# Kernel tuning notes

Hardware: AMD Instinct MI355X
Metric: run time of the kernel (lower is better)

## Reference

```python
import jax, jax.numpy as jnp
import numpy as np

N_NODES = 50000
N_EDGES = 800000
IN_DIM = 128
HIDDEN = 32
NHEAD = 4
OUT_DIM = 64
NEG_SLOPE = 0.2


def setup_inputs() -> dict:
    key = jax.random.key(0)
    ks = jax.random.split(key, 8)
    x = jax.random.normal(ks[0], (N_NODES, IN_DIM), dtype=jnp.float32)
    edge_index = jax.random.randint(ks[1], (2, N_EDGES), 0, N_NODES, dtype=jnp.int64)
    # layer 1: fc (in_dim -> nhead*hidden), attn [nhead, 2*hidden]
    W1 = jax.random.normal(ks[2], (IN_DIM, NHEAD * HIDDEN), dtype=jnp.float32) * 0.1
    attn1 = jax.random.normal(ks[3], (NHEAD, 2 * HIDDEN), dtype=jnp.float32) * 0.1
    # layer 2: fc (nhead*hidden -> 1*out_dim), attn [1, 2*out_dim]
    W2 = jax.random.normal(ks[4], (NHEAD * HIDDEN, OUT_DIM), dtype=jnp.float32) * 0.1
    attn2 = jax.random.normal(ks[5], (1, 2 * OUT_DIM), dtype=jnp.float32) * 0.1
    # extra output head: Linear(out_dim, out_dim) with bias
    head_W = jax.random.normal(ks[6], (OUT_DIM, OUT_DIM), dtype=jnp.float32) * 0.1
    head_b = jax.random.normal(ks[7], (OUT_DIM,), dtype=jnp.float32) * 0.1
    return {"x": x, "edge_index": edge_index, "W1": W1, "attn1": attn1,
            "W2": W2, "attn2": attn2, "head_W": head_W, "head_b": head_b}


def _gat_layer(x, W, attn, row, col, num_nodes, heads):
    """One GATConv: linear proj, edge attention, segment softmax over dst (col), scatter-add."""
    f_out = W.shape[1] // heads
    h = (x @ W).reshape(num_nodes, heads, f_out)            # [N, H, F]
    a_l, a_r = attn[:, :f_out], attn[:, f_out:]              # split attn for src/dst parts
    e_src = jnp.einsum('nhf,hf->nh', h, a_l)                 # [N, H]
    e_dst = jnp.einsum('nhf,hf->nh', h, a_r)                 # [N, H]
    alpha = e_src[row] + e_dst[col]                          # [E, H] == cat(h[row],h[col])·attn
    alpha = jax.nn.leaky_relu(alpha, NEG_SLOPE)
    # segment softmax grouped by destination node (col); self-loops guarantee non-empty segs
    amax = jax.ops.segment_max(alpha, col, num_segments=num_nodes)
    ex = jnp.exp(alpha - amax[col])
    denom = jax.ops.segment_sum(ex, col, num_segments=num_nodes)
    a = ex / denom[col]                                      # [E, H]
    msg = h[row] * a[:, :, None]                             # [E, H, F]
    out = jax.ops.segment_sum(msg, col, num_segments=num_nodes)  # [N, H, F]
    return out.reshape(num_nodes, heads * f_out)


def reference(x, edge_index, W1, attn1, W2, attn2, head_W, head_b):
    n = x.shape[0]
    loops = jnp.arange(n, dtype=edge_index.dtype)
    row = jnp.concatenate([edge_index[0], loops])
    col = jnp.concatenate([edge_index[1], loops])
    h = _gat_layer(x, W1, attn1, row, col, n, NHEAD)         # [N, NHEAD*HIDDEN]
    h = jax.nn.relu(h)                                       # intermediate-layer activation
    h = _gat_layer(h, W2, attn2, row, col, n, 1)             # [N, OUT_DIM] (last: no act)
    out = h @ head_W + head_b                                # extra_output_fc head
    return out
```

## Files before the change

### kernel.cpp

```cpp
#include <hip/hip_runtime.h>
#include <math.h>

#define N_NODES 50000
#define E_RAW 800000
#define E_TOT 850000
#define NEG_SLOPE 0.2f
#define G1_BLOCKS ((N_NODES + 63) / 64)
#define NBUCK 391
#define EPB 2048
#define PBLK ((E_TOT + EPB - 1) / EPB)

typedef __attribute__((ext_vector_type(8))) short bf16x8;
typedef __attribute__((ext_vector_type(4))) float f32x4;

__device__ __forceinline__ float lrelu(float a) { return a > 0.f ? a : NEG_SLOPE * a; }

__device__ __forceinline__ unsigned f2bf(float f) {
    unsigned u = __float_as_uint(f);
    return (u + 0x7fff + ((u >> 16) & 1)) >> 16;
}
__device__ __forceinline__ unsigned pack2(float a, float b) {
    return f2bf(a) | (f2bf(b) << 16);
}
__device__ __forceinline__ float bflo(unsigned p) { return __uint_as_float(p << 16); }
__device__ __forceinline__ float bfhi(unsigned p) { return __uint_as_float(p & 0xffff0000u); }

__global__ void k_prepB(const float* __restrict__ W, unsigned* __restrict__ Btg) {
    int c = blockIdx.x;
    int tq = threadIdx.x;
    float a = W[(2 * tq) * 128 + c];
    float b = W[(2 * tq + 1) * 128 + c];
    Btg[c * 64 + tq] = pack2(a, b);
}

__global__ void k_gemm1_p1(const float* __restrict__ A, const unsigned* __restrict__ Btg,
                           const float* __restrict__ aux, uint2* __restrict__ C,
                           float* __restrict__ es, float* __restrict__ ed,
                           const int* __restrict__ ei, int* __restrict__ hist2d) {
    __shared__ unsigned As[64 * 64];
    if (blockIdx.x >= G1_BLOCKS) {
        int blk = blockIdx.x - G1_BLOCKS;
        int* h = (int*)As;
        for (int i = threadIdx.x; i < NBUCK; i += 256) h[i] = 0;
        __syncthreads();
        int base = blk * EPB;
        for (int i = threadIdx.x; i < EPB; i += 256) {
            int e = base + i;
            if (e >= E_TOT) break;
            int col = (e < E_RAW) ? ei[E_RAW + e] : (e - E_RAW);
            atomicAdd(&h[col >> 7], 1);
        }
        __syncthreads();
        for (int i = threadIdx.x; i < NBUCK; i += 256) hist2d[i * PBLK + blk] = h[i];
        return;
    }
    int t = threadIdx.x;
    int m0 = blockIdx.x * 64;
    int rows = min(64, N_NODES - m0);
    const float4* A4 = (const float4*)(A + (size_t)m0 * 128);
    for (int i = t; i < rows * 32; i += 256) {
        int row = i >> 5, k4 = i & 31;
        float4 v = A4[i];
        int byte = (k4 * 8) ^ ((row & 7) << 4);
        unsigned* p = &As[row * 64 + (byte >> 2)];
        p[0] = pack2(v.x, v.y);
        p[1] = pack2(v.z, v.w);
    }
    __syncthreads();
    int lane = t & 63, wave = t >> 6;
    int r15 = lane & 15, g = lane >> 4;
    int arow = wave * 16 + r15;
    f32x4 acc[8];
#pragma unroll
    for (int i = 0; i < 8; ++i) acc[i] = (f32x4){0.f, 0.f, 0.f, 0.f};
    const char* Abase = (const char*)As + arow * 256;
    int swz = (arow & 7) << 4;
    const char* Bbase = (const char*)Btg;
#pragma unroll
    for (int s = 0; s < 4; ++s) {
        bf16x8 xf = *(const bf16x8*)(Abase + ((64 * s + 16 * g) ^ swz));
#pragma unroll
        for (int tt = 0; tt < 8; ++tt) {
            bf16x8 wf = *(const bf16x8*)(Bbase + ((16 * tt + r15) * 256 + 64 * s + 16 * g));
            acc[tt] = __builtin_amdgcn_mfma_f32_16x16x32_bf16(wf, xf, acc[tt], 0, 0, 0);
        }
    }
    int grow = m0 + arow;
    bool valid = (arow < rows);
    if (valid) {
        uint2* C2 = C + (size_t)grow * 32;
#pragma unroll
        for (int tt = 0; tt < 8; ++tt) {
            uint2 v; v.x = pack2(acc[tt][0], acc[tt][1]); v.y = pack2(acc[tt][2], acc[tt][3]);
            C2[4 * tt + g] = v;
        }
    }
    float ps0 = 0.f, ps1 = 0.f, ps2 = 0.f, ps3 = 0.f;
    float pd0 = 0.f, pd1 = 0.f, pd2 = 0.f, pd3 = 0.f;
#pragma unroll
    for (int tt = 0; tt < 8; ++tt) {
        int h = tt >> 1;
        int fin = 16 * (tt & 1) + 4 * g;
        float4 alv = *(const float4*)(aux + h * 64 + fin);
        float4 arv = *(const float4*)(aux + h * 64 + 32 + fin);
        float s4 = acc[tt][0] * alv.x + acc[tt][1] * alv.y + acc[tt][2] * alv.z + acc[tt][3] * alv.w;
        float d4 = acc[tt][0] * arv.x + acc[tt][1] * arv.y + acc[tt][2] * arv.z + acc[tt][3] * arv.w;
        if (h == 0) { ps0 += s4; pd0 += d4; }
        else if (h == 1) { ps1 += s4; pd1 += d4; }
        else if (h == 2) { ps2 += s4; pd2 += d4; }
        else { ps3 += s4; pd3 += d4; }
    }
#pragma unroll
    for (int mask = 16; mask <= 32; mask <<= 1) {
        ps0 += __shfl_xor(ps0, mask); ps1 += __shfl_xor(ps1, mask);
        ps2 += __shfl_xor(ps2, mask); ps3 += __shfl_xor(ps3, mask);
        pd0 += __shfl_xor(pd0, mask); pd1 += __shfl_xor(pd1, mask);
        pd2 += __shfl_xor(pd2, mask); pd3 += __shfl_xor(pd3, mask);
    }
    if (valid) {
        float psg = (g == 0) ? ps0 : (g == 1) ? ps1 : (g == 2) ? ps2 : ps3;
        float pdg = (g == 0) ? pd0 : (g == 1) ? pd1 : (g == 2) ? pd2 : pd3;
        es[grow * 4 + g] = psg;
        ed[grow * 4 + g] = pdg;
    }
}

__global__ void k_p2a(const int* __restrict__ hist2d, int* __restrict__ off2d,
                      int* __restrict__ bucktot) {
    __shared__ int sh[512];
    int b = blockIdx.x, t = threadIdx.x;
    int v = (t < PBLK) ? hist2d[b * PBLK + t] : 0;
    sh[t] = v;
    __syncthreads();
    for (int ofs = 1; ofs < 512; ofs <<= 1) {
        int u = (t >= ofs) ? sh[t - ofs] : 0;
        __syncthreads();
        sh[t] += u;
        __syncthreads();
    }
    if (t < PBLK) off2d[b * PBLK + t] = sh[t] - v;
    if (t == 511) bucktot[b] = sh[511];
}

__global__ void k_p2b(const int* __restrict__ bucktot, int* __restrict__ bucketbase) {
    __shared__ int sh[512];
    int t = threadIdx.x;
    int v = (t < NBUCK) ? bucktot[t] : 0;
    sh[t] = v;
    __syncthreads();
    for (int ofs = 1; ofs < 512; ofs <<= 1) {
        int u = (t >= ofs) ? sh[t - ofs] : 0;
        __syncthreads();
        sh[t] += u;
        __syncthreads();
    }
    if (t < NBUCK) bucketbase[t] = sh[t] - v;
    if (t == 511) bucketbase[NBUCK] = sh[511];
}

__global__ void k_p3(const int* __restrict__ ei, const int* __restrict__ off2d,
                     const int* __restrict__ bucketbase, unsigned* __restrict__ part) {
    __shared__ int h[NBUCK];
    __shared__ int basebuf[NBUCK];
    int blk = blockIdx.x, t = threadIdx.x;
    for (int i = t; i < NBUCK; i += 256) {
        h[i] = 0;
        basebuf[i] = bucketbase[i] + off2d[i * PBLK + blk];
    }
    __syncthreads();
    int base = blk * EPB;
    for (int i = t; i < EPB; i += 256) {
        int e = base + i;
        if (e >= E_TOT) break;
        int col, src;
        if (e < E_RAW) { col = ei[E_RAW + e]; src = ei[e]; }
        else { col = src = e - E_RAW; }
        int b = col >> 7;
        int lr = atomicAdd(&h[b], 1);
        part[basebuf[b] + lr] = (unsigned)src | ((unsigned)(col & 127) << 16);
    }
}

__global__ void k_p4(const unsigned* __restrict__ part, const int* __restrict__ bucketbase,
                     int* __restrict__ off, unsigned short* __restrict__ srcs) {
    __shared__ int h[128];
    __shared__ int colofs[128];
    int b = blockIdx.x, t = threadIdx.x;
    int s0 = bucketbase[b], s1 = bucketbase[b + 1];
    if (t < 128) h[t] = 0;
    __syncthreads();
    for (int i = s0 + t; i < s1; i += 256) atomicAdd(&h[part[i] >> 16], 1);
    __syncthreads();
    if (t == 0) {
        int acc = 0;
        for (int c = 0; c < 128; ++c) { colofs[c] = acc; acc += h[c]; }
    }
    __syncthreads();
    int colbase = b * 128, ncols = min(128, N_NODES - colbase);
    if (t < ncols) off[colbase + t] = s0 + colofs[t];
    if (b == NBUCK - 1 && t == 0) off[N_NODES] = s1;
    if (t < 128) h[t] = colofs[t];
    __syncthreads();
    for (int i = s0 + t; i < s1; i += 256) {
        unsigned u = part[i];
        int c = u >> 16;
        int slot = atomicAdd(&h[c], 1);
        srcs[s0 + slot] = (unsigned short)(u & 0xffffu);
    }
}

template<int K, int EPI>
__global__ void k_gemm23(const float* __restrict__ A, const float* __restrict__ B,
                         const float* __restrict__ aux, void* __restrict__ Cv,
                         float* __restrict__ es, float* __restrict__ ed) {
    constexpr int MT = 32;
    __shared__ float As[MT * K];
    int m0 = blockIdx.x * MT;
    int t = threadIdx.x, g = t >> 4, l = t & 15;
    int rows = min(MT, N_NODES - m0);
    const float4* A4 = (const float4*)(A + (size_t)m0 * K);
    float4* S4 = (float4*)As;
    for (int i = t; i < rows * (K / 4); i += 64) S4[i] = A4[i];
    __syncthreads();
    float acc[8][4];
#pragma unroll
    for (int r = 0; r < 8; ++r)
#pragma unroll
        for (int c = 0; c < 4; ++c) acc[r][c] = 0.f;
    const float4* B4 = (const float4*)B;
    for (int kk = 0; kk < K / 4; ++kk) {
        float4 b0 = B4[(4 * kk + 0) * 16 + l];
        float4 b1 = B4[(4 * kk + 1) * 16 + l];
        float4 b2 = B4[(4 * kk + 2) * 16 + l];
        float4 b3 = B4[(4 * kk + 3) * 16 + l];
#pragma unroll
        for (int r = 0; r < 8; ++r) {
            float4 a = ((const float4*)(As + (g * 8 + r) * K))[kk];
            acc[r][0] = fmaf(a.x, b0.x, fmaf(a.y, b1.x, fmaf(a.z, b2.x, fmaf(a.w, b3.x, acc[r][0]))));
            acc[r][1] = fmaf(a.x, b0.y, fmaf(a.y, b1.y, fmaf(a.z, b2.y, fmaf(a.w, b3.y, acc[r][1]))));
            acc[r][2] = fmaf(a.x, b0.z, fmaf(a.y, b1.z, fmaf(a.z, b2.z, fmaf(a.w, b3.z, acc[r][2]))));
            acc[r][3] = fmaf(a.x, b0.w, fmaf(a.y, b1.w, fmaf(a.z, b2.w, fmaf(a.w, b3.w, acc[r][3]))));
        }
    }
    if (EPI == 2) {
        uint2* C = (uint2*)Cv;
        float al0 = aux[4 * l], al1 = aux[4 * l + 1], al2 = aux[4 * l + 2], al3 = aux[4 * l + 3];
        float ar0 = aux[64 + 4 * l], ar1 = aux[64 + 4 * l + 1], ar2 = aux[64 + 4 * l + 2], ar3 = aux[64 + 4 * l + 3];
#pragma unroll
        for (int r = 0; r < 8; ++r) {
            int row = m0 + g * 8 + r;
            float pl = acc[r][0] * al0 + acc[r][1] * al1 + acc[r][2] * al2 + acc[r][3] * al3;
            float pr = acc[r][0] * ar0 + acc[r][1] * ar1 + acc[r][2] * ar2 + acc[r][3] * ar3;
#pragma unroll
            for (int mask = 8; mask; mask >>= 1) { pl += __shfl_xor(pl, mask); pr += __shfl_xor(pr, mask); }
            if (row < N_NODES) {
                uint2 v; v.x = pack2(acc[r][0], acc[r][1]); v.y = pack2(acc[r][2], acc[r][3]);
                C[(size_t)row * 16 + l] = v;
                if (l == 0) { es[row] = pl; ed[row] = pr; }
            }
        }
    } else {
        float4* C = (float4*)Cv;
        float4 bv = ((const float4*)aux)[l];
#pragma unroll
        for (int r = 0; r < 8; ++r) {
            int row = m0 + g * 8 + r;
            if (row < N_NODES) {
                float4 v;
                v.x = acc[r][0] + bv.x; v.y = acc[r][1] + bv.y;
                v.z = acc[r][2] + bv.z; v.w = acc[r][3] + bv.w;
                C[(size_t)row * 16 + l] = v;
            }
        }
    }
}

__global__ void k_agg1(const unsigned* __restrict__ h1b, const float* __restrict__ es,
                       const float* __restrict__ ed, const int* __restrict__ off,
                       const unsigned short* __restrict__ srcs, float* __restrict__ out1) {
    int n = blockIdx.x * (blockDim.x >> 6) + (threadIdx.x >> 6);
    int lane = threadIdx.x & 63;
    if (n >= N_NODES) return;
    int myh = lane & 3;
    float edh = ed[n * 4 + myh];
    int hc = lane >> 4;
    int s = off[n], e = off[n + 1];
    int jj = lane >> 2;
    float ax = 0.f, ay = 0.f, psum = 0.f;
    for (int base = s; base < e; base += 16) {
        int cnt = e - base;
        int srcj = 0;
        float w = 0.f;
        if (jj < cnt) {
            srcj = srcs[base + jj];
            w = __expf(lrelu(es[srcj * 4 + myh] + edh));
        }
        psum += w;
        unsigned pv[16];
        float wv[16];
#pragma unroll
        for (int j2 = 0; j2 < 16; ++j2) {
            int src = __shfl(srcj, j2 * 4);
            wv[j2] = __shfl(w, j2 * 4 + hc);
            pv[j2] = h1b[(size_t)src * 64 + lane];
        }
#pragma unroll
        for (int j2 = 0; j2 < 16; ++j2) {
            ax = fmaf(bflo(pv[j2]), wv[j2], ax);
            ay = fmaf(bfhi(pv[j2]), wv[j2], ay);
        }
    }
#pragma unroll
    for (int mask = 4; mask <= 32; mask <<= 1) psum += __shfl_xor(psum, mask);
    float inv = 1.f / __shfl(psum, hc);
    float2 o;
    o.x = fmaxf(ax * inv, 0.f);
    o.y = fmaxf(ay * inv, 0.f);
    ((float2*)out1)[(size_t)n * 64 + lane] = o;
}

__global__ void k_agg2(const unsigned* __restrict__ h2b, const float* __restrict__ es,
                       const float* __restrict__ ed, const int* __restrict__ off,
                       const unsigned short* __restrict__ srcs, float* __restrict__ outv) {
    int n = blockIdx.x * (blockDim.x >> 5) + (threadIdx.x >> 5);
    int l = threadIdx.x & 31;
    int hb = threadIdx.x & 32;
    if (n >= N_NODES) return;
    float edv = ed[n];
    int s = off[n], e = off[n + 1];
    const uint2* gp = (const uint2*)h2b;
    int l16 = l & 15;
    int sb0 = (l >> 4) * 2;
    float a0 = 0.f, a1 = 0.f, a2 = 0.f, a3 = 0.f, psum = 0.f;
    for (int base = s; base < e; base += 32) {
        int cnt = e - base;
        int srcj = 0;
        float w = 0.f;
        if (l < cnt) {
            srcj = srcs[base + l];
            w = __expf(lrelu(es[srcj] + edv));
        }
        psum += w;
#pragma unroll
        for (int sub = 0; sub < 2; ++sub) {
            uint2 pv[8];
            float wv[8];
#pragma unroll
            for (int j = 0; j < 8; ++j) {
                int lsrc = hb + (sb0 + sub) * 8 + j;
                int src = __shfl(srcj, lsrc);
                wv[j] = __shfl(w, lsrc);
                pv[j] = gp[(size_t)src * 16 + l16];
            }
#pragma unroll
            for (int j = 0; j < 8; ++j) {
                a0 = fmaf(bflo(pv[j].x), wv[j], a0);
                a1 = fmaf(bfhi(pv[j].x), wv[j], a1);
                a2 = fmaf(bflo(pv[j].y), wv[j], a2);
                a3 = fmaf(bfhi(pv[j].y), wv[j], a3);
            }
        }
    }
#pragma unroll
    for (int mask = 1; mask <= 16; mask <<= 1) psum += __shfl_xor(psum, mask);
    float inv = 1.f / psum;
    a0 += __shfl_xor(a0, 16); a1 += __shfl_xor(a1, 16);
    a2 += __shfl_xor(a2, 16); a3 += __shfl_xor(a3, 16);
    if (l < 16) {
        float4 o;
        o.x = a0 * inv; o.y = a1 * inv; o.z = a2 * inv; o.w = a3 * inv;
        ((float4*)outv)[(size_t)n * 16 + l16] = o;
    }
}

extern "C" void kernel_launch(void* const* d_in, const int* in_sizes, int n_in,
                              void* d_out, int out_size, void* d_ws, size_t ws_size,
                              hipStream_t stream) {
    const float* x     = (const float*)d_in[0];
    const int*   ei    = (const int*)d_in[1];
    const float* W1    = (const float*)d_in[2];
    const float* attn1 = (const float*)d_in[3];
    const float* W2    = (const float*)d_in[4];
    const float* attn2 = (const float*)d_in[5];
    const float* headW = (const float*)d_in[6];
    const float* headb = (const float*)d_in[7];
    float* out = (float*)d_out;

    char* ws = (char*)d_ws;
    size_t o = 0;
    auto alloc = [&](size_t bytes) -> void* {
        o = (o + 255) & ~(size_t)255;
        void* p = ws + o;
        o += bytes;
        return p;
    };
    unsigned*       h1b    = (unsigned*)alloc((size_t)N_NODES * 128 * 2);
    float*          out1   = (float*)alloc((size_t)N_NODES * 128 * 4);
    unsigned*       h2b    = (unsigned*)alloc((size_t)N_NODES * 64 * 2);
    float*          h2agg  = (float*)alloc((size_t)N_NODES * 64 * 4);
    float*          e1s    = (float*)alloc((size_t)N_NODES * 4 * 4);
    float*          e1d    = (float*)alloc((size_t)N_NODES * 4 * 4);
    float*          e2s    = (float*)alloc((size_t)N_NODES * 4);
    float*          e2d    = (float*)alloc((size_t)N_NODES * 4);
    int*            off    = (int*)alloc((size_t)(N_NODES + 1) * 4);
    unsigned short* srcs   = (unsigned short*)alloc((size_t)E_TOT * 2);
    unsigned*       Btg    = (unsigned*)alloc((size_t)128 * 64 * 4);
    int*            hist2d = (int*)alloc((size_t)NBUCK * PBLK * 4);
    int*            off2d  = (int*)alloc((size_t)NBUCK * PBLK * 4);
    int*            bucktot = (int*)alloc((size_t)NBUCK * 4);
    int*            bucketbase = (int*)alloc((size_t)(NBUCK + 1) * 4);
    unsigned*       part   = (unsigned*)alloc((size_t)E_TOT * 4);

    k_prepB<<<128, 64, 0, stream>>>(W1, Btg);

    k_gemm1_p1<<<G1_BLOCKS + PBLK, 256, 0, stream>>>(
        x, Btg, attn1, (uint2*)h1b, e1s, e1d, ei, hist2d);

    k_p2a<<<NBUCK, 512, 0, stream>>>(hist2d, off2d, bucktot);
    k_p2b<<<1, 512, 0, stream>>>(bucktot, bucketbase);
    k_p3<<<PBLK, 256, 0, stream>>>(ei, off2d, bucketbase, part);
    k_p4<<<NBUCK, 256, 0, stream>>>(part, bucketbase, off, srcs);

    k_agg1<<<N_NODES / 4, 256, 0, stream>>>(h1b, e1s, e1d, off, srcs, out1);

    k_gemm23<128, 2><<<(N_NODES + 31) / 32, 64, 0, stream>>>(out1, W2, attn2, h2b, e2s, e2d);
    k_agg2<<<N_NODES / 8, 256, 0, stream>>>(h2b, e2s, e2d, off, srcs, h2agg);

    k_gemm23<64, 3><<<(N_NODES + 31) / 32, 64, 0, stream>>>(h2agg, headW, headb, out, nullptr, nullptr);
}
```

Measured before the change: 238.5 us.

## Use bf16 MFMA for layer-2 GEMM with bf16 layer-1 output

Layer-1 aggregation now writes its ReLU output as packed bf16 instead of fp32, which halves that intermediate buffer. The layer-2 projection is replaced by an MFMA 16x16x32 bf16 kernel that stages rows in swizzled LDS, reads a pre-packed transposed W2 prepared alongside W1, and computes the attention logits in its epilogue. The aggregation loop also skips gathers for edges past the segment end. In exchange, layer-2 inputs lose precision to bf16 rounding.

```diff
diff --git a/kernel.cpp b/kernel.cpp
--- a/kernel.cpp
+++ b/kernel.cpp
@@ -25,12 +25,16 @@
 __device__ __forceinline__ float bflo(unsigned p) { return __uint_as_float(p << 16); }
 __device__ __forceinline__ float bfhi(unsigned p) { return __uint_as_float(p & 0xffff0000u); }
 
-__global__ void k_prepB(const float* __restrict__ W, unsigned* __restrict__ Btg) {
+__global__ void k_prep(const float* __restrict__ W1, const float* __restrict__ W2,
+                       unsigned* __restrict__ Btg, unsigned* __restrict__ B2tg) {
     int c = blockIdx.x;
     int tq = threadIdx.x;
-    float a = W[(2 * tq) * 128 + c];
-    float b = W[(2 * tq + 1) * 128 + c];
-    Btg[c * 64 + tq] = pack2(a, b);
+    if (c < 128) {
+        Btg[c * 64 + tq] = pack2(W1[(2 * tq) * 128 + c], W1[(2 * tq + 1) * 128 + c]);
+    } else {
+        int c2 = c - 128;
+        B2tg[c2 * 64 + tq] = pack2(W2[(2 * tq) * 64 + c2], W2[(2 * tq + 1) * 64 + c2]);
+    }
 }
 
 __global__ void k_gemm1_p1(const float* __restrict__ A, const unsigned* __restrict__ Btg,
@@ -209,11 +213,70 @@
     }
 }
 
-template<int K, int EPI>
-__global__ void k_gemm23(const float* __restrict__ A, const float* __restrict__ B,
-                         const float* __restrict__ aux, void* __restrict__ Cv,
+__global__ void k_gemm2m(const unsigned* __restrict__ A, const unsigned* __restrict__ B2tg,
+                         const float* __restrict__ aux, uint2* __restrict__ C,
                          float* __restrict__ es, float* __restrict__ ed) {
-    constexpr int MT = 32;
+    __shared__ unsigned As[64 * 64];
+    int t = threadIdx.x;
+    int m0 = blockIdx.x * 64;
+    int rows = min(64, N_NODES - m0);
+    const uint4* A4 = (const uint4*)(A + (size_t)m0 * 64);
+    for (int i = t; i < rows * 16; i += 256) {
+        int row = i >> 4, q = i & 15;
+        uint4 v = A4[i];
+        int byte = (q * 16) ^ ((row & 7) << 4);
+        unsigned* p = &As[row * 64 + (byte >> 2)];
+        p[0] = v.x; p[1] = v.y; p[2] = v.z; p[3] = v.w;
+    }
+    __syncthreads();
+    int lane = t & 63, wave = t >> 6;
+    int r15 = lane & 15, g = lane >> 4;
+    int arow = wave * 16 + r15;
+    f32x4 acc[4];
+#pragma unroll
+    for (int i = 0; i < 4; ++i) acc[i] = (f32x4){0.f, 0.f, 0.f, 0.f};
+    const char* Abase = (const char*)As + arow * 256;
+    int swz = (arow & 7) << 4;
+    const char* Bbase = (const char*)B2tg;
+#pragma unroll
+    for (int s = 0; s < 4; ++s) {
+        bf16x8 xf = *(const bf16x8*)(Abase + ((64 * s + 16 * g) ^ swz));
+#pragma unroll
+        for (int tt = 0; tt < 4; ++tt) {
+            bf16x8 wf = *(const bf16x8*)(Bbase + ((16 * tt + r15) * 256 + 64 * s + 16 * g));
+            acc[tt] = __builtin_amdgcn_mfma_f32_16x16x32_bf16(wf, xf, acc[tt], 0, 0, 0);
+        }
+    }
+    int grow = m0 + arow;
+    bool valid = (arow < rows);
+    if (valid) {
+        uint2* C2 = C + (size_t)grow * 16;
+#pragma unroll
+        for (int tt = 0; tt < 4; ++tt) {
+            uint2 v; v.x = pack2(acc[tt][0], acc[tt][1]); v.y = pack2(acc[tt][2], acc[tt][3]);
+            C2[4 * tt + g] = v;
+        }
+    }
+    float pl = 0.f, pr = 0.f;
+#pragma unroll
+    for (int tt = 0; tt < 4; ++tt) {
+        int f0 = 16 * tt + 4 * g;
+        float4 alv = *(const float4*)(aux + f0);
+        float4 arv = *(const float4*)(aux + 64 + f0);
+        pl += acc[tt][0] * alv.x + acc[tt][1] * alv.y + acc[tt][2] * alv.z + acc[tt][3] * alv.w;
+        pr += acc[tt][0] * arv.x + acc[tt][1] * arv.y + acc[tt][2] * arv.z + acc[tt][3] * arv.w;
+    }
+#pragma unroll
+    for (int mask = 16; mask <= 32; mask <<= 1) {
+        pl += __shfl_xor(pl, mask);
+        pr += __shfl_xor(pr, mask);
+    }
+    if (valid && g == 0) { es[grow] = pl; ed[grow] = pr; }
+}
+
+__global__ void k_head(const float* __restrict__ A, const float* __restrict__ B,
+                       const float* __restrict__ aux, float* __restrict__ Cv) {
+    constexpr int K = 64, MT = 32;
     __shared__ float As[MT * K];
     int m0 = blockIdx.x * MT;
     int t = threadIdx.x, g = t >> 4, l = t & 15;
@@ -242,42 +305,23 @@
             acc[r][3] = fmaf(a.x, b0.w, fmaf(a.y, b1.w, fmaf(a.z, b2.w, fmaf(a.w, b3.w, acc[r][3]))));
         }
     }
-    if (EPI == 2) {
-        uint2* C = (uint2*)Cv;
-        float al0 = aux[4 * l], al1 = aux[4 * l + 1], al2 = aux[4 * l + 2], al3 = aux[4 * l + 3];
-        float ar0 = aux[64 + 4 * l], ar1 = aux[64 + 4 * l + 1], ar2 = aux[64 + 4 * l + 2], ar3 = aux[64 + 4 * l + 3];
-#pragma unroll
-        for (int r = 0; r < 8; ++r) {
-            int row = m0 + g * 8 + r;
-            float pl = acc[r][0] * al0 + acc[r][1] * al1 + acc[r][2] * al2 + acc[r][3] * al3;
-            float pr = acc[r][0] * ar0 + acc[r][1] * ar1 + acc[r][2] * ar2 + acc[r][3] * ar3;
-#pragma unroll
-            for (int mask = 8; mask; mask >>= 1) { pl += __shfl_xor(pl, mask); pr += __shfl_xor(pr, mask); }
-            if (row < N_NODES) {
-                uint2 v; v.x = pack2(acc[r][0], acc[r][1]); v.y = pack2(acc[r][2], acc[r][3]);
-                C[(size_t)row * 16 + l] = v;
-                if (l == 0) { es[row] = pl; ed[row] = pr; }
-            }
-        }
-    } else {
-        float4* C = (float4*)Cv;
-        float4 bv = ((const float4*)aux)[l];
-#pragma unroll
-        for (int r = 0; r < 8; ++r) {
-            int row = m0 + g * 8 + r;
-            if (row < N_NODES) {
-                float4 v;
-                v.x = acc[r][0] + bv.x; v.y = acc[r][1] + bv.y;
-                v.z = acc[r][2] + bv.z; v.w = acc[r][3] + bv.w;
-                C[(size_t)row * 16 + l] = v;
-            }
+    float4* C = (float4*)Cv;
+    float4 bv = ((const float4*)aux)[l];
+#pragma unroll
+    for (int r = 0; r < 8; ++r) {
+        int row = m0 + g * 8 + r;
+        if (row < N_NODES) {
+            float4 v;
+            v.x = acc[r][0] + bv.x; v.y = acc[r][1] + bv.y;
+            v.z = acc[r][2] + bv.z; v.w = acc[r][3] + bv.w;
+            C[(size_t)row * 16 + l] = v;
         }
     }
 }
 
 __global__ void k_agg1(const unsigned* __restrict__ h1b, const float* __restrict__ es,
                        const float* __restrict__ ed, const int* __restrict__ off,
-                       const unsigned short* __restrict__ srcs, float* __restrict__ out1) {
+                       const unsigned short* __restrict__ srcs, unsigned* __restrict__ out1) {
     int n = blockIdx.x * (blockDim.x >> 6) + (threadIdx.x >> 6);
     int lane = threadIdx.x & 63;
     if (n >= N_NODES) return;
@@ -300,9 +344,13 @@
         float wv[16];
 #pragma unroll
         for (int j2 = 0; j2 < 16; ++j2) {
-            int src = __shfl(srcj, j2 * 4);
-            wv[j2] = __shfl(w, j2 * 4 + hc);
-            pv[j2] = h1b[(size_t)src * 64 + lane];
+            if (j2 < cnt) {
+                int src = __shfl(srcj, j2 * 4);
+                wv[j2] = __shfl(w, j2 * 4 + hc);
+                pv[j2] = h1b[(size_t)src * 64 + lane];
+            } else {
+                wv[j2] = 0.f; pv[j2] = 0u;
+            }
         }
 #pragma unroll
         for (int j2 = 0; j2 < 16; ++j2) {
@@ -313,10 +361,7 @@
 #pragma unroll
     for (int mask = 4; mask <= 32; mask <<= 1) psum += __shfl_xor(psum, mask);
     float inv = 1.f / __shfl(psum, hc);
-    float2 o;
-    o.x = fmaxf(ax * inv, 0.f);
-    o.y = fmaxf(ay * inv, 0.f);
-    ((float2*)out1)[(size_t)n * 64 + lane] = o;
+    out1[(size_t)n * 64 + lane] = pack2(fmaxf(ax * inv, 0.f), fmaxf(ay * inv, 0.f));
 }
 
 __global__ void k_agg2(const unsigned* __restrict__ h2b, const float* __restrict__ es,
@@ -395,7 +440,7 @@
         return p;
     };
     unsigned*       h1b    = (unsigned*)alloc((size_t)N_NODES * 128 * 2);
-    float*          out1   = (float*)alloc((size_t)N_NODES * 128 * 4);
+    unsigned*       out1b  = (unsigned*)alloc((size_t)N_NODES * 128 * 2);
     unsigned*       h2b    = (unsigned*)alloc((size_t)N_NODES * 64 * 2);
     float*          h2agg  = (float*)alloc((size_t)N_NODES * 64 * 4);
     float*          e1s    = (float*)alloc((size_t)N_NODES * 4 * 4);
@@ -405,13 +450,14 @@
     int*            off    = (int*)alloc((size_t)(N_NODES + 1) * 4);
     unsigned short* srcs   = (unsigned short*)alloc((size_t)E_TOT * 2);
     unsigned*       Btg    = (unsigned*)alloc((size_t)128 * 64 * 4);
+    unsigned*       B2tg   = (unsigned*)alloc((size_t)64 * 64 * 4);
     int*            hist2d = (int*)alloc((size_t)NBUCK * PBLK * 4);
     int*            off2d  = (int*)alloc((size_t)NBUCK * PBLK * 4);
     int*            bucktot = (int*)alloc((size_t)NBUCK * 4);
     int*            bucketbase = (int*)alloc((size_t)(NBUCK + 1) * 4);
     unsigned*       part   = (unsigned*)alloc((size_t)E_TOT * 4);
 
-    k_prepB<<<128, 64, 0, stream>>>(W1, Btg);
+    k_prep<<<192, 64, 0, stream>>>(W1, W2, Btg, B2tg);
 
     k_gemm1_p1<<<G1_BLOCKS + PBLK, 256, 0, stream>>>(
         x, Btg, attn1, (uint2*)h1b, e1s, e1d, ei, hist2d);
@@ -421,10 +467,10 @@
     k_p3<<<PBLK, 256, 0, stream>>>(ei, off2d, bucketbase, part);
     k_p4<<<NBUCK, 256, 0, stream>>>(part, bucketbase, off, srcs);
 
-    k_agg1<<<N_NODES / 4, 256, 0, stream>>>(h1b, e1s, e1d, off, srcs, out1);
-
-    k_gemm23<128, 2><<<(N_NODES + 31) / 32, 64, 0, stream>>>(out1, W2, attn2, h2b, e2s, e2d);
+    k_agg1<<<N_NODES / 4, 256, 0, stream>>>(h1b, e1s, e1d, off, srcs, out1b);
+
+    k_gemm2m<<<(N_NODES + 63) / 64, 256, 0, stream>>>(out1b, B2tg, attn2, (uint2*)h2b, e2s, e2d);
     k_agg2<<<N_NODES / 8, 256, 0, stream>>>(h2b, e2s, e2d, off, srcs, h2agg);
 
-    k_gemm23<64, 3><<<(N_NODES + 31) / 32, 64, 0, stream>>>(h2agg, headW, headb, out, nullptr, nullptr);
-}
+    k_head<<<(N_NODES + 31) / 32, 64, 0, stream>>>(h2agg, headW, headb, out);
+}
```

After: 222.4 us. 1.07x faster.
